# Kernel tuning notes

Measured on AMD Instinct MI355X. Metric: run time of the kernel, lower is better.

The kernel has to match this reference:

```python
import jax, jax.numpy as jnp
import numpy as np
import math

D_MODEL = 512
NUM_HEADS = 8
B, L = 2, 4096
EPS_NORM = 1e-8
PLASTICITY = 1.0


def setup_inputs() -> dict:
    key = jax.random.key(0)
    ks = jax.random.split(key, 6)
    D, H = D_MODEL, NUM_HEADS
    std = 1.0 / math.sqrt(D)
    x = jax.random.normal(ks[0], (B, L, D), dtype=jnp.float32)
    qkv_w = jax.random.normal(ks[1], (3 * D, D), dtype=jnp.float32) * std
    qkv_b = jnp.zeros((3 * D,), dtype=jnp.float32)
    out_w = jax.random.normal(ks[2], (D, D), dtype=jnp.float32) * std
    out_b = jnp.zeros((D,), dtype=jnp.float32)
    decay_w = jax.random.normal(ks[3], (H, D), dtype=jnp.float32) * 0.02
    decay_b = jnp.full((H,), 4.0, dtype=jnp.float32)
    norm_scale = jnp.ones((D,), dtype=jnp.float32)
    return {"x": x, "qkv_w": qkv_w, "qkv_b": qkv_b, "out_w": out_w,
            "out_b": out_b, "decay_w": decay_w, "decay_b": decay_b,
            "norm_scale": norm_scale}


def _hebbian_forward(x, qkv_w, qkv_b, out_w, out_b, decay_w, decay_b, norm_scale):
    Bsz, Lsz, D = x.shape
    H = NUM_HEADS
    E = D // H
    # QKV projection (torch Linear: y = x @ W.T + b)
    qkv = x @ qkv_w.T + qkv_b
    q, k, v = jnp.split(qkv, 3, axis=-1)
    q = q.reshape(Bsz, Lsz, H, E)
    k = k.reshape(Bsz, Lsz, H, E)
    v = v.reshape(Bsz, Lsz, H, E)
    # feature map: elu(x) + 1
    q = (jax.nn.elu(q) + 1.0) / math.sqrt(E)
    k = jax.nn.elu(k) + 1.0
    # input-dependent decay per head
    decay_logits = x @ decay_w.T + decay_b          # (B,L,H)
    lambdas = (0.9 + 0.1 * jax.nn.sigmoid(decay_logits)) * PLASTICITY
    log_lambdas = jnp.log(jnp.clip(lambdas, 1e-6))[..., None]   # (B,L,H,1)
    log_lambda_cum = jnp.clip(jnp.cumsum(log_lambdas, axis=1), -50.0, 50.0)
    decay_k = jnp.exp(-log_lambda_cum)
    decay_q = jnp.exp(log_lambda_cum)
    k_decayed = k * decay_k
    q_decayed = q * decay_q
    # outer-product memory state cumsum: (B,L,H,E,E)
    kv = jnp.einsum('blhe,blhf->blhef', k_decayed, v)
    memory_state = jnp.cumsum(kv, axis=1)
    k_sum_decayed = jnp.cumsum(k_decayed, axis=1)
    num = jnp.einsum('blhe,blhef->blhf', q_decayed, memory_state)
    den = jnp.einsum('blhe,blhe->blh', q_decayed, k_sum_decayed)[..., None] + 1e-6
    out = (num / den).reshape(Bsz, Lsz, D)
    out = out @ out_w.T + out_b
    # RMSNorm (dropout is identity in eval)
    rnorm = jax.lax.rsqrt(jnp.mean(out * out, axis=-1, keepdims=True) + EPS_NORM)
    return out * rnorm * norm_scale


def reference(x, qkv_w, qkv_b, out_w, out_b, decay_w, decay_b, norm_scale):
    return _hebbian_forward(x, qkv_w, qkv_b, out_w, out_b, decay_w, decay_b, norm_scale)
```

## Files before the change

kernel.cpp:

```cpp
#include <hip/hip_runtime.h>

typedef unsigned short u16;
typedef unsigned int u32;

#define B_ 2
#define L_ 4096
#define D_ 512
#define H_ 8
#define E_ 64
#define M_ (B_*L_)
#define TD (3*D_)
#define NCH (L_/64)
#define BH (B_*H_)

typedef short bf16x8 __attribute__((ext_vector_type(8)));
typedef float f32x4 __attribute__((ext_vector_type(4)));

__device__ __forceinline__ float bf2f(u16 u){ return __uint_as_float(((u32)u)<<16); }
__device__ __forceinline__ u16 f2bf(float f){
  u32 u = __float_as_uint(f);
  u32 r = u + 0x7FFFu + ((u>>16)&1u);
  return (u16)(r>>16);
}
__device__ __forceinline__ float elu1(float v){ return v>0.f ? v+1.f : __expf(v); }

__device__ __forceinline__ void async_ld16(const u16* g, u16* l){
  __builtin_amdgcn_global_load_lds(
      (const __attribute__((address_space(1))) void*)g,
      (__attribute__((address_space(3))) void*)l, 16, 0, 0);
}

__global__ __launch_bounds__(256) void decay_conv_kernel(const float* __restrict__ x,
    const float* __restrict__ dw, const float* __restrict__ db,
    const float* __restrict__ qw, const float* __restrict__ ow,
    float* __restrict__ ll, u16* __restrict__ xb,
    u16* __restrict__ qwb, u16* __restrict__ owb)
{
  int blk = blockIdx.x;
  if (blk < 2048){
    int wv = threadIdx.x>>6, lane = threadIdx.x&63;
    int m = blk*4 + wv;
    float xr[8];
    #pragma unroll
    for (int i=0;i<8;i++) xr[i] = x[(size_t)m*D_ + lane + 64*i];
    #pragma unroll
    for (int i=0;i<8;i++) xb[(size_t)m*D_ + lane + 64*i] = f2bf(xr[i]);
    int b = m >> 12, l = m & (L_-1);
    for (int h=0; h<H_; h++){
      float acc = 0.f;
      #pragma unroll
      for (int i=0;i<8;i++) acc += xr[i]*dw[h*D_ + lane + 64*i];
      #pragma unroll
      for (int off=32; off>0; off>>=1) acc += __shfl_xor(acc, off);
      if (lane == h){
        float z = acc + db[h];
        float lam = 0.9f + 0.1f/(1.f + __expf(-z));
        ll[((b*H_+h)*L_) + l] = logf(lam);
      }
    }
  } else {
    int gid = (blk-2048)*256 + threadIdx.x;
    const float* src; u16* dst; int off;
    if (gid < 196608){ src = qw; dst = qwb; off = gid; }
    else { src = ow; dst = owb; off = gid - 196608; }
    float4 v = ((const float4*)src)[off];
    ushort4 o; o.x=f2bf(v.x); o.y=f2bf(v.y); o.z=f2bf(v.z); o.w=f2bf(v.w);
    ((ushort4*)dst)[off] = o;
  }
}

__global__ __launch_bounds__(256) void scan_kernel(const float* __restrict__ ll,
    float* __restrict__ cb)
{
  int bh = blockIdx.x, t = threadIdx.x;
  int lane = t & 63, wv = t >> 6;
  const float* p = ll + (size_t)bh*L_ + t*16;
  float s[16];
  #pragma unroll
  for (int q=0;q<4;q++){
    float4 v = *(const float4*)(p + q*4);
    s[q*4+0]=v.x; s[q*4+1]=v.y; s[q*4+2]=v.z; s[q*4+3]=v.w;
  }
  #pragma unroll
  for (int i=1;i<16;i++) s[i] += s[i-1];
  float tot = s[15];
  float ws = tot;
  #pragma unroll
  for (int off=1; off<64; off<<=1){
    float tmp = __shfl_up(ws, off);
    if (lane >= off) ws += tmp;
  }
  __shared__ float wsum[4];
  if (lane == 63) wsum[wv] = ws;
  __syncthreads();
  float base = 0.f;
  #pragma unroll
  for (int w2=0; w2<3; w2++) if (w2 < wv) base += wsum[w2];
  float ex = base + ws - tot;
  float* c = cb + (size_t)bh*L_ + t*16;
  #pragma unroll
  for (int i=0;i<16;i++) c[i] = fminf(50.f, fmaxf(-50.f, ex + s[i]));
}

template<bool OB>
__global__ __launch_bounds__(256) void gemm_mfma(const u16* __restrict__ A,
    const u16* __restrict__ W, const float* __restrict__ bias,
    void* __restrict__ Cv, int M, int N, int K)
{
  __shared__ u16 As[128*32];
  __shared__ u16 Bs[128*32];
  int n0 = blockIdx.x*128, m0 = blockIdx.y*128;
  int t = threadIdx.x, wave = t>>6, lane = t&63;
  int wm = (wave>>1)*64, wn = (wave&1)*64;
  f32x4 acc[4][4] = {};
  int srow = wave*32 + (lane>>2);
  int scol = (lane&3)*8;
  const u16* gA = A + (size_t)(m0+srow)*K + scol;
  const u16* gB = W + (size_t)(n0+srow)*K + scol;
  u16* lA = As + wave*1024;
  u16* lB = Bs + wave*1024;
  int q8 = (lane>>4)*8, r16 = lane&15;
  for (int k0=0; k0<K; k0+=32){
    async_ld16(gA + k0,                lA);
    async_ld16(gA + k0 + 16*(size_t)K, lA + 512);
    async_ld16(gB + k0,                lB);
    async_ld16(gB + k0 + 16*(size_t)K, lB + 512);
    __syncthreads();
    bf16x8 af[4], bfr[4];
    #pragma unroll
    for (int i=0;i<4;i++) af[i]  = *(const bf16x8*)&As[(wm + i*16 + r16)*32 + q8];
    #pragma unroll
    for (int j=0;j<4;j++) bfr[j] = *(const bf16x8*)&Bs[(wn + j*16 + r16)*32 + q8];
    #pragma unroll
    for (int i=0;i<4;i++)
      #pragma unroll
      for (int j=0;j<4;j++)
        acc[i][j] = __builtin_amdgcn_mfma_f32_16x16x32_bf16(af[i], bfr[j], acc[i][j], 0,0,0);
    __syncthreads();
  }
  #pragma unroll
  for (int i=0;i<4;i++){
    int row = m0 + wm + i*16 + (lane>>4)*4;
    #pragma unroll
    for (int j=0;j<4;j++){
      int col = n0 + wn + j*16 + r16;
      float bv = bias[col];
      #pragma unroll
      for (int r=0;r<4;r++){
        float val = acc[i][j][r] + bv;
        if (OB) ((u16*)Cv)[(size_t)(row+r)*N + col] = f2bf(val);
        else    ((float*)Cv)[(size_t)(row+r)*N + col] = val;
      }
    }
  }
}

__global__ __launch_bounds__(256) void transform_sums_kernel(const u16* __restrict__ qkvb,
    const float* __restrict__ cb, u16* __restrict__ qc, u16* __restrict__ kc,
    u16* __restrict__ vtc, u16* __restrict__ Stc, float* __restrict__ ksc)
{
  int bid = blockIdx.x;
  int bh = bid >> 6, ch = bid & 63;
  int b = bh >> 3, h = bh & 7;
  __shared__ u16 Ks[64*72];
  __shared__ u16 Vs[64*72];
  __shared__ u16 Ktl[128*40];
  __shared__ u16 Vtl[128*40];
  __shared__ float ksr[256];
  int t = threadIdx.x;
  size_t mbase = (size_t)b*L_ + ch*64;
  #pragma unroll
  for (int i=0;i<2;i++){
    int idx = t + 256*i;
    int l = idx>>3, e0 = (idx&7)*8;
    int kh = e0>>5, ej = e0&31;
    float c = cb[(size_t)bh*L_ + ch*64 + l];
    float eqc = __expf(c)*0.125f, ekc = __expf(-c);
    const u16* src = qkvb + (mbase+l)*TD + h*64 + e0;
    union { uint4 v; u16 s[8]; } in, o;
    in.v = *(const uint4*)src;
    #pragma unroll
    for (int j=0;j<8;j++) o.s[j] = f2bf(elu1(bf2f(in.s[j]))*eqc);
    *(uint4*)(qc + ((size_t)bid*2 + kh)*2048 + l*32 + ej) = o.v;
    in.v = *(const uint4*)(src + D_);
    #pragma unroll
    for (int j=0;j<8;j++) o.s[j] = f2bf(elu1(bf2f(in.s[j]))*ekc);
    *(uint4*)(kc + ((size_t)bid*2 + kh)*2048 + l*32 + ej) = o.v;
    *(uint4*)&Ks[l*72+e0] = o.v;
    *(uint4*)&Vs[l*72+e0] = *(const uint4*)(src + 2*D_);
  }
  __syncthreads();
  int e = t & 63, jq = t >> 6;
  {
    u16 kv[16] __attribute__((aligned(16)));
    u16 vv[16] __attribute__((aligned(16)));
    float ksum = 0.f;
    #pragma unroll
    for (int jj=0;jj<16;jj++){
      int j = jq*16+jj;
      kv[jj] = Ks[j*72 + e];
      ksum += bf2f(kv[jj]);
      vv[jj] = Vs[j*72 + e];
    }
    int kh = jq>>1, jl = (jq&1)*16;
    u16* kt = &Ktl[(kh*64 + e)*40 + jl];
    u16* vt = &Vtl[(kh*64 + e)*40 + jl];
    *(uint4*)kt     = *(const uint4*)&kv[0];
    *(uint4*)(kt+8) = *(const uint4*)&kv[8];
    *(uint4*)vt     = *(const uint4*)&vv[0];
    *(uint4*)(vt+8) = *(const uint4*)&vv[8];
    ksr[t] = ksum;
  }
  __syncthreads();
  {
    int row = t>>1, c0 = (t&1)*16;
    *(uint4*)&vtc[(size_t)bid*4096 + row*32 + c0]     = *(const uint4*)&Vtl[row*40 + c0];
    *(uint4*)&vtc[(size_t)bid*4096 + row*32 + c0 + 8] = *(const uint4*)&Vtl[row*40 + c0 + 8];
  }
  int w = t>>6, lane = t&63;
  int r16 = lane & 15, q8 = (lane>>4)*8;
  bf16x8 av[2];
  #pragma unroll
  for (int kh=0;kh<2;kh++)
    av[kh] = *(const bf16x8*)&Vtl[(kh*64 + w*16 + r16)*40 + q8];
  f32x4 acc[4] = {};
  #pragma unroll
  for (int et=0;et<4;et++)
    #pragma unroll
    for (int kh=0;kh<2;kh++){
      bf16x8 bv = *(const bf16x8*)&Ktl[(kh*64 + et*16 + r16)*40 + q8];
      acc[et] = __builtin_amdgcn_mfma_f32_16x16x32_bf16(av[kh], bv, acc[et], 0,0,0);
    }
  #pragma unroll
  for (int et=0;et<4;et++){
    int eh = et>>1, el = (et&1)*16 + r16;
    #pragma unroll
    for (int r=0;r<4;r++){
      int f = w*16 + (lane>>4)*4 + r;
      Stc[((size_t)bid*2 + eh)*2048 + f*32 + el] = f2bf(acc[et][r]);
    }
  }
  if (t < 64) ksc[bid*64 + t] = ksr[t] + ksr[64+t] + ksr[128+t] + ksr[192+t];
}

__global__ __launch_bounds__(256) void chunk_prefix_kernel(u16* __restrict__ Stc,
    float* __restrict__ ksc)
{
  int blk = blockIdx.x, t = threadIdx.x;
  if (blk < 128){
    int gid = blk*256 + t;
    int bh = gid >> 11, e2 = gid & 2047;
    u32* p = (u32*)Stc + (size_t)bh*131072 + e2;
    float r0 = 0.f, r1 = 0.f;
    #pragma unroll 8
    for (int ch=0; ch<NCH; ch++){
      u32 v = p[ch*2048];
      float lo = bf2f((u16)(v & 0xffffu));
      float hi = bf2f((u16)(v >> 16));
      p[ch*2048] = (u32)f2bf(r0) | ((u32)f2bf(r1) << 16);
      r0 += lo; r1 += hi;
    }
  } else {
    int gid2 = (blk-128)*256 + t;
    int bh2 = gid2 >> 6, e = gid2 & 63;
    float* kp = ksc + bh2*4096 + e;
    float kr = 0.f;
    #pragma unroll 8
    for (int ch=0; ch<NCH; ch++){
      float v = kp[ch*64]; kp[ch*64] = kr; kr += v;
    }
  }
}

__global__ __launch_bounds__(256) void chunk_out_kernel(const u16* __restrict__ qc,
    const u16* __restrict__ kc, const u16* __restrict__ vtc,
    const u16* __restrict__ Stc, const float* __restrict__ ksc,
    u16* __restrict__ attn)
{
  int bid = blockIdx.x;
  int bh = bid >> 6, ch = bid & 63;
  int b = bh >> 3, h = bh & 7;
  __shared__ u16 KV[16384];
  __shared__ u16 Ab[4096];
  __shared__ float kp[64], den4[256], den[64];
  int t = threadIdx.x, w = t>>6, lane = t&63;
  size_t mbase = (size_t)b*L_ + ch*64;
  const u16* srcs[4] = { qc, kc, vtc, Stc };
  {
    const u16* gbase = srcs[w] + (size_t)bid*4096 + lane*8;
    #pragma unroll
    for (int q=0;q<8;q++)
      async_ld16(gbase + q*512, KV + w*4096 + q*512);
  }
  if (t < 64) kp[t] = ksc[bid*64 + t];
  __syncthreads();
  const u16* Qs   = KV;
  const u16* Kb_s = KV + 4096;
  const u16* Vt_s = KV + 8192;
  const u16* St_s = KV + 12288;
  int r16 = lane & 15, q8 = (lane>>4)*8;
  bf16x8 aq[2];
  #pragma unroll
  for (int eh=0;eh<2;eh++)
    aq[eh] = *(const bf16x8*)&Qs[(eh*64 + w*16 + r16)*32 + q8];
  f32x4 accA[4] = {};
  #pragma unroll
  for (int jt=0;jt<4;jt++)
    #pragma unroll
    for (int eh=0;eh<2;eh++){
      bf16x8 bv = *(const bf16x8*)&Kb_s[(eh*64 + jt*16 + r16)*32 + q8];
      accA[jt] = __builtin_amdgcn_mfma_f32_16x16x32_bf16(aq[eh], bv, accA[jt], 0,0,0);
    }
  int l4 = t>>2, q4 = t&3;
  float dkp = 0.f;
  {
    int eh = q4>>1, el0 = (q4&1)*16;
    bf16x8 x1 = *(const bf16x8*)&Qs[(eh*64 + l4)*32 + el0];
    bf16x8 x2 = *(const bf16x8*)&Qs[(eh*64 + l4)*32 + el0 + 8];
    #pragma unroll
    for (int i=0;i<8;i++)
      dkp += bf2f((u16)x1[i])*kp[q4*16+i] + bf2f((u16)x2[i])*kp[q4*16+8+i];
  }
  #pragma unroll
  for (int jt=0;jt<4;jt++)
    #pragma unroll
    for (int r=0;r<4;r++){
      int lr = w*16 + ((lane>>4)<<2) + r;
      int j  = jt*16 + r16;
      Ab[((jt>>1)*64 + lr)*32 + (jt&1)*16 + r16] = (j <= lr) ? f2bf(accA[jt][r]) : (u16)0;
    }
  __syncthreads();
  float dA = 0.f;
  {
    int jh2 = q4>>1, jl0 = (q4&1)*16;
    bf16x8 y1 = *(const bf16x8*)&Ab[(jh2*64 + l4)*32 + jl0];
    bf16x8 y2 = *(const bf16x8*)&Ab[(jh2*64 + l4)*32 + jl0 + 8];
    #pragma unroll
    for (int i=0;i<8;i++) dA += bf2f((u16)y1[i]) + bf2f((u16)y2[i]);
  }
  den4[t] = dkp + dA;
  __syncthreads();
  if (t < 64) den[t] = den4[t*4] + den4[t*4+1] + den4[t*4+2] + den4[t*4+3] + 1e-6f;
  bf16x8 aA[2];
  #pragma unroll
  for (int jh=0;jh<2;jh++)
    aA[jh] = *(const bf16x8*)&Ab[(jh*64 + w*16 + r16)*32 + q8];
  f32x4 acc[4] = {};
  #pragma unroll
  for (int ft=0;ft<4;ft++){
    #pragma unroll
    for (int jh=0;jh<2;jh++){
      bf16x8 bv = *(const bf16x8*)&Vt_s[(jh*64 + ft*16 + r16)*32 + q8];
      acc[ft] = __builtin_amdgcn_mfma_f32_16x16x32_bf16(aA[jh], bv, acc[ft], 0,0,0);
    }
    #pragma unroll
    for (int eh=0;eh<2;eh++){
      bf16x8 bv = *(const bf16x8*)&St_s[(eh*64 + ft*16 + r16)*32 + q8];
      acc[ft] = __builtin_amdgcn_mfma_f32_16x16x32_bf16(aq[eh], bv, acc[ft], 0,0,0);
    }
  }
  __syncthreads();
  float inv[4];
  #pragma unroll
  for (int r=0;r<4;r++) inv[r] = 1.f / den[w*16 + ((lane>>4)<<2) + r];
  #pragma unroll
  for (int ft=0;ft<4;ft++)
    #pragma unroll
    for (int r=0;r<4;r++){
      int lr = w*16 + ((lane>>4)<<2) + r;
      attn[(mbase + lr)*D_ + h*64 + ft*16 + r16] = f2bf(acc[ft][r]*inv[r]);
    }
}

__global__ __launch_bounds__(256) void gemm_rms_kernel(const u16* __restrict__ A,
    const u16* __restrict__ W, const float* __restrict__ bias,
    const float* __restrict__ gnorm, float* __restrict__ out)
{
  __shared__ u16 As[32*32];
  __shared__ u16 Bs[512*32];
  __shared__ float ssq_l[4][32];
  __shared__ float rinv_l[32];
  int m0 = blockIdx.x*32;
  int t = threadIdx.x, wave = t>>6, lane = t&63;
  int wn = wave*128;
  int r16 = lane&15, q8 = (lane>>4)*8;
  f32x4 acc[2][8] = {};
  int scol = (t&3)*8;
  const u16* gB = W + (size_t)(t>>2)*512 + scol;
  const u16* gA = A + (size_t)(m0 + (t>>2))*512 + scol;
  u16* lB = Bs + wave*512;
  u16* lA = As + wave*512;
  for (int k0=0; k0<512; k0+=32){
    if (wave < 2) async_ld16(gA + k0, lA);
    #pragma unroll
    for (int it=0; it<8; it++)
      async_ld16(gB + k0 + it*32768, lB + it*2048);
    __syncthreads();
    bf16x8 af[2];
    af[0] = *(const bf16x8*)&As[r16*32 + q8];
    af[1] = *(const bf16x8*)&As[(16 + r16)*32 + q8];
    #pragma unroll
    for (int j=0;j<8;j++){
      bf16x8 bv = *(const bf16x8*)&Bs[(wn + j*16 + r16)*32 + q8];
      acc[0][j] = __builtin_amdgcn_mfma_f32_16x16x32_bf16(af[0], bv, acc[0][j], 0,0,0);
      acc[1][j] = __builtin_amdgcn_mfma_f32_16x16x32_bf16(af[1], bv, acc[1][j], 0,0,0);
    }
    __syncthreads();
  }
  int g = lane>>4;
  float bv8[8], gv8[8];
  #pragma unroll
  for (int j=0;j<8;j++){ int col = wn + j*16 + r16; bv8[j] = bias[col]; gv8[j] = gnorm[col]; }
  float ssq[2][4] = {};
  #pragma unroll
  for (int i=0;i<2;i++)
    #pragma unroll
    for (int j=0;j<8;j++)
      #pragma unroll
      for (int r=0;r<4;r++){
        float v = acc[i][j][r] + bv8[j];
        acc[i][j][r] = v;
        ssq[i][r] += v*v;
      }
  #pragma unroll
  for (int off=1; off<16; off<<=1)
    #pragma unroll
    for (int i=0;i<2;i++)
      #pragma unroll
      for (int r=0;r<4;r++)
        ssq[i][r] += __shfl_xor(ssq[i][r], off);
  if (r16 == 0){
    #pragma unroll
    for (int i=0;i<2;i++)
      #pragma unroll
      for (int r=0;r<4;r++)
        ssq_l[wave][i*16 + g*4 + r] = ssq[i][r];
  }
  __syncthreads();
  if (t < 32)
    rinv_l[t] = rsqrtf((ssq_l[0][t]+ssq_l[1][t]+ssq_l[2][t]+ssq_l[3][t])*(1.f/512.f) + 1e-8f);
  __syncthreads();
  #pragma unroll
  for (int i=0;i<2;i++)
    #pragma unroll
    for (int r=0;r<4;r++){
      int row = m0 + i*16 + g*4 + r;
      float ri = rinv_l[i*16 + g*4 + r];
      #pragma unroll
      for (int j=0;j<8;j++)
        out[(size_t)row*512 + wn + j*16 + r16] = acc[i][j][r]*ri*gv8[j];
    }
}

extern "C" void kernel_launch(void* const* d_in, const int* in_sizes, int n_in,
                              void* d_out, int out_size, void* d_ws, size_t ws_size,
                              hipStream_t stream)
{
  const float* x     = (const float*)d_in[0];
  const float* w_qkv = (const float*)d_in[1];
  const float* b_qkv = (const float*)d_in[2];
  const float* w_out = (const float*)d_in[3];
  const float* b_out = (const float*)d_in[4];
  const float* w_dec = (const float*)d_in[5];
  const float* b_dec = (const float*)d_in[6];
  const float* gnorm = (const float*)d_in[7];
  float* out = (float*)d_out;

  char* ws = (char*)d_ws;
  u16*   qkvb = (u16*)(ws);
  u16*   qc   = (u16*)(ws + 25165824);
  u16*   kc   = (u16*)(ws + 33554432);
  u16*   vtc  = (u16*)(ws + 41943040);
  u16*   Stc  = (u16*)(ws + 50331648);
  float* ksc  = (float*)(ws + 58720256);
  float* ll   = (float*)(ws + 58982400);
  float* cb   = (float*)(ws + 59244544);
  u16*   xb   = (u16*)(ws + 59506688);
  u16*   qwb  = (u16*)(ws + 67895296);
  u16*   owb  = (u16*)(ws + 69468160);
  u16*   attn = xb;

  decay_conv_kernel<<<dim3(3072), dim3(256), 0, stream>>>(x, w_dec, b_dec, w_qkv, w_out,
                                                          ll, xb, qwb, owb);
  scan_kernel<<<dim3(BH), dim3(256), 0, stream>>>(ll, cb);
  gemm_mfma<true><<<dim3(TD/128, M_/128), dim3(256), 0, stream>>>(xb, qwb, b_qkv, qkvb, M_, TD, D_);
  transform_sums_kernel<<<dim3(BH*NCH), dim3(256), 0, stream>>>(qkvb, cb, qc, kc, vtc, Stc, ksc);
  chunk_prefix_kernel<<<dim3(132), dim3(256), 0, stream>>>(Stc, ksc);
  chunk_out_kernel<<<dim3(BH*NCH), dim3(256), 0, stream>>>(qc, kc, vtc, Stc, ksc, attn);
  gemm_rms_kernel<<<dim3(M_/32), dim3(256), 0, stream>>>(attn, owb, b_out, gnorm, out);
}
```

Baseline: 160.8 us.

## Double-buffer LDS tiles in GEMMs and batch decay head reductions

Both bf16 MFMA GEMM kernels (the QKV projection and the output projection fused with RMSNorm) now use two shared-memory buffers. Each iteration prefetches the next K-slice asynchronously while MFMAs run on the current one, and one barrier per iteration replaces two, so global-load latency overlaps with compute. The cost is double the LDS footprint, which may reduce occupancy, especially in the RMS kernel with its large 512-row B tile. The decay-logit kernel replaces eight separate full-wave shuffle reductions with a butterfly transpose-reduce that sums all eight heads with fewer shuffles, and uses fast __logf. There are also minor tweaks: an unroll bump in the chunk prefix scan and a select instead of a pointer array for load sources.

After: 156.0 us. -3.0%, faster.

```diff
diff --git a/kernel.cpp b/kernel.cpp
--- a/kernel.cpp
+++ b/kernel.cpp
@@ -46,17 +46,46 @@
     #pragma unroll
     for (int i=0;i<8;i++) xb[(size_t)m*D_ + lane + 64*i] = f2bf(xr[i]);
     int b = m >> 12, l = m & (L_-1);
-    for (int h=0; h<H_; h++){
-      float acc = 0.f;
-      #pragma unroll
-      for (int i=0;i<8;i++) acc += xr[i]*dw[h*D_ + lane + 64*i];
-      #pragma unroll
-      for (int off=32; off>0; off>>=1) acc += __shfl_xor(acc, off);
-      if (lane == h){
-        float z = acc + db[h];
-        float lam = 0.9f + 0.1f/(1.f + __expf(-z));
-        ll[((b*H_+h)*L_) + l] = logf(lam);
-      }
+    float acc8[8];
+    #pragma unroll
+    for (int h=0; h<8; h++){
+      float a = 0.f;
+      #pragma unroll
+      for (int i=0;i<8;i++) a += xr[i]*dw[h*D_ + lane + 64*i];
+      acc8[h] = a;
+    }
+    float s4[4];
+    #pragma unroll
+    for (int i=0;i<4;i++){
+      float a = acc8[2*i], bb = acc8[2*i+1];
+      bool odd = lane & 1;
+      float keep = odd ? bb : a;
+      float send = odd ? a : bb;
+      s4[i] = keep + __shfl_xor(send, 1);
+    }
+    float s2[2];
+    #pragma unroll
+    for (int j=0;j<2;j++){
+      float a = s4[2*j], bb = s4[2*j+1];
+      bool sel = (lane>>1) & 1;
+      float keep = sel ? bb : a;
+      float send = sel ? a : bb;
+      s2[j] = keep + __shfl_xor(send, 2);
+    }
+    float r;
+    {
+      bool sel = (lane>>2) & 1;
+      float keep = sel ? s2[1] : s2[0];
+      float send = sel ? s2[0] : s2[1];
+      r = keep + __shfl_xor(send, 4);
+    }
+    r += __shfl_xor(r, 8);
+    r += __shfl_xor(r, 16);
+    r += __shfl_xor(r, 32);
+    if (lane < 8){
+      float z = r + db[lane];
+      float lam = 0.9f + 0.1f/(1.f + __expf(-z));
+      ll[((b*H_+lane)*L_) + l] = __logf(lam);
     }
   } else {
     int gid = (blk-2048)*256 + threadIdx.x;
@@ -107,8 +136,8 @@
     const u16* __restrict__ W, const float* __restrict__ bias,
     void* __restrict__ Cv, int M, int N, int K)
 {
-  __shared__ u16 As[128*32];
-  __shared__ u16 Bs[128*32];
+  __shared__ u16 As[2][128*32];
+  __shared__ u16 Bs[2][128*32];
   int n0 = blockIdx.x*128, m0 = blockIdx.y*128;
   int t = threadIdx.x, wave = t>>6, lane = t&63;
   int wm = (wave>>1)*64, wn = (wave&1)*64;
@@ -117,26 +146,39 @@
   int scol = (lane&3)*8;
   const u16* gA = A + (size_t)(m0+srow)*K + scol;
   const u16* gB = W + (size_t)(n0+srow)*K + scol;
-  u16* lA = As + wave*1024;
-  u16* lB = Bs + wave*1024;
   int q8 = (lane>>4)*8, r16 = lane&15;
+  {
+    u16* lA = As[0] + wave*1024;
+    u16* lB = Bs[0] + wave*1024;
+    async_ld16(gA,                lA);
+    async_ld16(gA + 16*(size_t)K, lA + 512);
+    async_ld16(gB,                lB);
+    async_ld16(gB + 16*(size_t)K, lB + 512);
+  }
+  __syncthreads();
+  int cur = 0;
+  #pragma unroll 2
   for (int k0=0; k0<K; k0+=32){
-    async_ld16(gA + k0,                lA);
-    async_ld16(gA + k0 + 16*(size_t)K, lA + 512);
-    async_ld16(gB + k0,                lB);
-    async_ld16(gB + k0 + 16*(size_t)K, lB + 512);
-    __syncthreads();
+    if (k0 + 32 < K){
+      u16* lA = As[cur^1] + wave*1024;
+      u16* lB = Bs[cur^1] + wave*1024;
+      async_ld16(gA + k0+32,                lA);
+      async_ld16(gA + k0+32 + 16*(size_t)K, lA + 512);
+      async_ld16(gB + k0+32,                lB);
+      async_ld16(gB + k0+32 + 16*(size_t)K, lB + 512);
+    }
     bf16x8 af[4], bfr[4];
     #pragma unroll
-    for (int i=0;i<4;i++) af[i]  = *(const bf16x8*)&As[(wm + i*16 + r16)*32 + q8];
-    #pragma unroll
-    for (int j=0;j<4;j++) bfr[j] = *(const bf16x8*)&Bs[(wn + j*16 + r16)*32 + q8];
+    for (int i=0;i<4;i++) af[i]  = *(const bf16x8*)&As[cur][(wm + i*16 + r16)*32 + q8];
+    #pragma unroll
+    for (int j=0;j<4;j++) bfr[j] = *(const bf16x8*)&Bs[cur][(wn + j*16 + r16)*32 + q8];
     #pragma unroll
     for (int i=0;i<4;i++)
       #pragma unroll
       for (int j=0;j<4;j++)
         acc[i][j] = __builtin_amdgcn_mfma_f32_16x16x32_bf16(af[i], bfr[j], acc[i][j], 0,0,0);
     __syncthreads();
+    cur ^= 1;
   }
   #pragma unroll
   for (int i=0;i<4;i++){
@@ -252,7 +294,7 @@
     int bh = gid >> 11, e2 = gid & 2047;
     u32* p = (u32*)Stc + (size_t)bh*131072 + e2;
     float r0 = 0.f, r1 = 0.f;
-    #pragma unroll 8
+    #pragma unroll 16
     for (int ch=0; ch<NCH; ch++){
       u32 v = p[ch*2048];
       float lo = bf2f((u16)(v & 0xffffu));
@@ -285,9 +327,9 @@
   __shared__ float kp[64], den4[256], den[64];
   int t = threadIdx.x, w = t>>6, lane = t&63;
   size_t mbase = (size_t)b*L_ + ch*64;
-  const u16* srcs[4] = { qc, kc, vtc, Stc };
-  {
-    const u16* gbase = srcs[w] + (size_t)bid*4096 + lane*8;
+  const u16* gsrc = (w==0) ? qc : (w==1) ? kc : (w==2) ? vtc : Stc;
+  {
+    const u16* gbase = gsrc + (size_t)bid*4096 + lane*8;
     #pragma unroll
     for (int q=0;q<8;q++)
       async_ld16(gbase + q*512, KV + w*4096 + q*512);
@@ -376,8 +418,8 @@
     const u16* __restrict__ W, const float* __restrict__ bias,
     const float* __restrict__ gnorm, float* __restrict__ out)
 {
-  __shared__ u16 As[32*32];
-  __shared__ u16 Bs[512*32];
+  __shared__ u16 As[2][32*32];
+  __shared__ u16 Bs[2][512*32];
   __shared__ float ssq_l[4][32];
   __shared__ float rinv_l[32];
   int m0 = blockIdx.x*32;
@@ -388,24 +430,32 @@
   int scol = (t&3)*8;
   const u16* gB = W + (size_t)(t>>2)*512 + scol;
   const u16* gA = A + (size_t)(m0 + (t>>2))*512 + scol;
-  u16* lB = Bs + wave*512;
-  u16* lA = As + wave*512;
+  {
+    if (wave < 2) async_ld16(gA, As[0] + wave*512);
+    #pragma unroll
+    for (int it=0; it<8; it++)
+      async_ld16(gB + it*32768, Bs[0] + wave*512 + it*2048);
+  }
+  __syncthreads();
+  int cur = 0;
+  #pragma unroll 2
   for (int k0=0; k0<512; k0+=32){
-    if (wave < 2) async_ld16(gA + k0, lA);
-    #pragma unroll
-    for (int it=0; it<8; it++)
-      async_ld16(gB + k0 + it*32768, lB + it*2048);
+    if (k0 < 480){
+      if (wave < 2) async_ld16(gA + k0+32, As[cur^1] + wave*512);
+      #pragma unroll
+      for (int it=0; it<8; it++)
+        async_ld16(gB + k0+32 + it*32768, Bs[cur^1] + wave*512 + it*2048);
+    }
+    bf16x8 af0 = *(const bf16x8*)&As[cur][r16*32 + q8];
+    bf16x8 af1 = *(const bf16x8*)&As[cur][(16 + r16)*32 + q8];
+    #pragma unroll
+    for (int j=0;j<8;j++){
+      bf16x8 bv = *(const bf16x8*)&Bs[cur][(wn + j*16 + r16)*32 + q8];
+      acc[0][j] = __builtin_amdgcn_mfma_f32_16x16x32_bf16(af0, bv, acc[0][j], 0,0,0);
+      acc[1][j] = __builtin_amdgcn_mfma_f32_16x16x32_bf16(af1, bv, acc[1][j], 0,0,0);
+    }
     __syncthreads();
-    bf16x8 af[2];
-    af[0] = *(const bf16x8*)&As[r16*32 + q8];
-    af[1] = *(const bf16x8*)&As[(16 + r16)*32 + q8];
-    #pragma unroll
-    for (int j=0;j<8;j++){
-      bf16x8 bv = *(const bf16x8*)&Bs[(wn + j*16 + r16)*32 + q8];
-      acc[0][j] = __builtin_amdgcn_mfma_f32_16x16x32_bf16(af[0], bv, acc[0][j], 0,0,0);
-      acc[1][j] = __builtin_amdgcn_mfma_f32_16x16x32_bf16(af[1], bv, acc[1][j], 0,0,0);
-    }
-    __syncthreads();
+    cur ^= 1;
   }
   int g = lane>>4;
   float bv8[8], gv8[8];
```
